# Performance work log

Hardware: AMD Instinct MI355X
Metric: run time of the kernel (lower is better)

Reference implementation:

```python
import jax, jax.numpy as jnp
import numpy as np

GROUPS = 8
EPS = 1e-5


def group_norm(x, gamma, beta):
    # x: [B, C, H, W]; normalize per group over (C/g, H, W)
    B, C, H, W = x.shape
    xg = x.reshape(B, GROUPS, C // GROUPS, H, W)
    mean = xg.mean(axis=(2, 3, 4), keepdims=True)
    var = xg.var(axis=(2, 3, 4), keepdims=True)
    xg = (xg - mean) * jax.lax.rsqrt(var + EPS)
    x = xg.reshape(B, C, H, W)
    return x * gamma[None, :, None, None] + beta[None, :, None, None]


def setup_inputs() -> dict:
    key = jax.random.key(0)
    ks = jax.random.split(key, 6)
    B, C, H, W = 8, 512, 32, 32
    x = jax.random.normal(ks[0], (B, C, H, W), dtype=jnp.float32)
    gn_w = jnp.ones((C,), dtype=jnp.float32)
    gn_b = jnp.zeros((C,), dtype=jnp.float32)
    s = 1.0 / np.sqrt(C)
    qkv_w = jax.random.uniform(ks[1], (3 * C, C), minval=-s, maxval=s, dtype=jnp.float32)
    qkv_b = jax.random.uniform(ks[2], (3 * C,), minval=-s, maxval=s, dtype=jnp.float32)
    proj_w = jax.random.uniform(ks[3], (C, C), minval=-s, maxval=s, dtype=jnp.float32)
    proj_b = jax.random.uniform(ks[4], (C,), minval=-s, maxval=s, dtype=jnp.float32)
    return {"x": x, "gn_w": gn_w, "gn_b": gn_b, "qkv_w": qkv_w,
            "qkv_b": qkv_b, "proj_w": proj_w, "proj_b": proj_b}


def reference(x, gn_w, gn_b, qkv_w, qkv_b, proj_w, proj_b):
    B, C, H, W = x.shape
    xn = group_norm(x, gn_w, gn_b)              # [B,C,H,W] (also the residual)
    xf = xn.reshape(B, C, H * W).transpose(0, 2, 1)  # [B,N,C]
    qkv = jnp.einsum('bnc,dc->bnd', xf, qkv_w) + qkv_b  # [B,N,3C]
    q, k, v = jnp.split(qkv, 3, axis=-1)
    k = jax.nn.softmax(k, axis=-1)              # over channels
    q = jax.nn.softmax(q, axis=-2)              # over tokens
    context = jnp.einsum('bnc,bnd->bcd', k, v)  # [B,C,C]
    out = jnp.einsum('bnc,bcd->bnd', q, context)  # [B,N,C]
    out = jnp.einsum('bnc,dc->bnd', out, proj_w) + proj_b
    out = out.transpose(0, 2, 1).reshape(B, C, H, W)
    return out + xn
```

## Files before the change

### kernel.cpp

```cpp
#include <hip/hip_runtime.h>
#include <hip/hip_bf16.h>
#include <stdint.h>

typedef unsigned short u16;
typedef __attribute__((ext_vector_type(8))) short s16x8;
typedef __attribute__((ext_vector_type(4))) float f32x4;
typedef __attribute__((ext_vector_type(4))) unsigned short u16x4;

static constexpr int B_ = 8, C_ = 512, N_ = 1024, G_ = 8;
static constexpr float EPS = 1e-5f;

static constexpr size_t OFF_XNT  = 0;
static constexpr size_t OFF_Q    = OFF_XNT  + (size_t)B_*N_*C_*2;
static constexpr size_t OFF_K    = OFF_Q    + (size_t)B_*N_*C_*2;
static constexpr size_t OFF_V    = OFF_K    + (size_t)B_*N_*C_*2;
static constexpr size_t OFF_KT   = OFF_V    + (size_t)B_*N_*C_*2;
static constexpr size_t OFF_VT   = OFF_KT   + (size_t)B_*N_*C_*2;
static constexpr size_t OFF_QS   = OFF_VT   + (size_t)B_*N_*C_*2;
static constexpr size_t OFF_CTX  = OFF_QS   + (size_t)B_*N_*C_*2;
static constexpr size_t OFF_MT   = OFF_CTX  + (size_t)B_*C_*C_*2;
static constexpr size_t OFF_WQ   = OFF_MT   + (size_t)B_*C_*C_*2;
static constexpr size_t OFF_WP   = OFF_WQ   + (size_t)3*C_*C_*2;
static constexpr size_t OFF_GNP  = OFF_WP   + (size_t)C_*C_*2;

__device__ __forceinline__ float b2f(u16 u) {
  union { float f; uint32_t i; } x; x.i = ((uint32_t)u) << 16; return x.f;
}
__device__ __forceinline__ u16 f2b(float f) {
  union { float f; uint32_t i; } x; x.f = f;
  return (u16)((x.i + 0x7fffu + ((x.i >> 16) & 1u)) >> 16);
}
#define AS1 __attribute__((address_space(1)))
#define AS3 __attribute__((address_space(3)))
__device__ __forceinline__ void gl2lds16(const void* g, void* l) {
  __builtin_amdgcn_global_load_lds((const AS1 void*)g, (AS3 void*)l, 16, 0, 0);
}

__global__ __launch_bounds__(256) void gn_partial(const float* __restrict__ x,
                                                  float* __restrict__ gnp) {
  int bg = blockIdx.x;
  int chunk = blockIdx.y;
  const float4* p = reinterpret_cast<const float4*>(x + (size_t)bg * 65536 + (size_t)chunk * 8192);
  int tid = threadIdx.x;
  float s = 0.f, sq = 0.f;
#pragma unroll
  for (int i = 0; i < 8; ++i) {
    float4 v = p[i * 256 + tid];
    s  += v.x + v.y + v.z + v.w;
    sq += v.x*v.x + v.y*v.y + v.z*v.z + v.w*v.w;
  }
  for (int off = 32; off; off >>= 1) { s += __shfl_xor(s, off); sq += __shfl_xor(sq, off); }
  __shared__ float red[8];
  int wid = tid >> 6, lane = tid & 63;
  if (lane == 0) { red[wid*2] = s; red[wid*2+1] = sq; }
  __syncthreads();
  if (tid == 0) {
    gnp[(bg*8 + chunk)*2 + 0] = red[0]+red[2]+red[4]+red[6];
    gnp[(bg*8 + chunk)*2 + 1] = red[1]+red[3]+red[5]+red[7];
  }
}

__global__ __launch_bounds__(256) void gn_apply(const float* __restrict__ x,
                                                const float* __restrict__ gw,
                                                const float* __restrict__ gb,
                                                const float* __restrict__ gnp,
                                                u16* __restrict__ xnT) {
  __shared__ float T[64][65];
  int b = blockIdx.x, c0 = blockIdx.y * 64, n0 = blockIdx.z * 64;
  int bg = b * G_ + blockIdx.y;
  float S = 0.f, SQ = 0.f;
#pragma unroll
  for (int i = 0; i < 8; ++i) { S += gnp[(bg*8+i)*2]; SQ += gnp[(bg*8+i)*2+1]; }
  float mean = S * (1.f/65536.f);
  float var  = SQ * (1.f/65536.f) - mean*mean;
  float rstd = rsqrtf(var + EPS);
  int tn = threadIdx.x & 63, tc = threadIdx.x >> 6;
#pragma unroll 4
  for (int it = 0; it < 16; ++it) {
    int cl = it*4 + tc;
    int c = c0 + cl;
    float v = x[((size_t)b*C_ + c)*N_ + n0 + tn];
    T[tn][cl] = (v - mean) * rstd * gw[c] + gb[c];
  }
  __syncthreads();
#pragma unroll
  for (int p = 0; p < 2; ++p) {
    int nl = p*32 + (threadIdx.x >> 3);
    int cs = (threadIdx.x & 7) * 8;
    s16x8 o;
#pragma unroll
    for (int j = 0; j < 8; ++j) o[j] = (short)f2b(T[nl][cs + j]);
    *reinterpret_cast<s16x8*>(&xnT[((size_t)(b*N_ + n0 + nl))*C_ + c0 + cs]) = o;
  }
}

__global__ __launch_bounds__(256) void cvt_w2(const float* __restrict__ w1,
                                              const float* __restrict__ w2,
                                              u16* __restrict__ o1,
                                              u16* __restrict__ o2) {
  int i = blockIdx.x * 256 + threadIdx.x;
  const int n1 = 1536*512/4;
  if (i < n1) {
    float4 v = reinterpret_cast<const float4*>(w1)[i];
    u16x4 r = { f2b(v.x), f2b(v.y), f2b(v.z), f2b(v.w) };
    reinterpret_cast<u16x4*>(o1)[i] = r;
  } else {
    int j = i - n1;
    float4 v = reinterpret_cast<const float4*>(w2)[j];
    u16x4 r = { f2b(v.x), f2b(v.y), f2b(v.z), f2b(v.w) };
    reinterpret_cast<u16x4*>(o2)[j] = r;
  }
}

template<int BM, int BN, int EPI>
__global__ __launch_bounds__(256) void gemm(const u16* __restrict__ A,
                                            const u16* __restrict__ Bm,
                                            int M, int N, int K, int lda, int ldb,
                                            long strideA, long strideB, long strideC,
                                            const float* __restrict__ bias,
                                            void* __restrict__ O0,
                                            const void* __restrict__ R) {
  constexpr int BK = 64;
  constexpr int MI = BM / 32, NI = BN / 32;
  __shared__ u16 As[2][BM*BK];
  __shared__ u16 Bs[2][BN*BK];
  int tid = threadIdx.x, wid = tid >> 6, lane = tid & 63;
  int m0 = blockIdx.x * BM, n0 = blockIdx.y * BN;
  const u16* Ab = A + (size_t)strideA * blockIdx.z;
  const u16* Bp = Bm + (size_t)strideB * blockIdx.z;

  f32x4 acc[MI][NI] = {};
  int wm = (wid >> 1) * (BM/2), wn = (wid & 1) * (BN/2);
  int sr = lane >> 3;
  int sg = (lane & 7) ^ sr;

  auto stage = [&](int buf, int k0) {
#pragma unroll
    for (int t = 0; t < BM/32; ++t) {
      int chunk = wid*(BM/32) + t;
      gl2lds16(Ab + (size_t)(m0 + chunk*8 + sr)*lda + k0 + sg*8,
               (void*)(&As[buf][chunk*512]));
    }
#pragma unroll
    for (int t = 0; t < BN/32; ++t) {
      int chunk = wid*(BN/32) + t;
      gl2lds16(Bp + (size_t)(n0 + chunk*8 + sr)*ldb + k0 + sg*8,
               (void*)(&Bs[buf][chunk*512]));
    }
  };

  int KT = K / BK;
  stage(0, 0);
  __syncthreads();
  int cur = 0;
  for (int kt = 0; kt < KT; ++kt) {
    if (kt + 1 < KT) stage(cur ^ 1, (kt + 1) * BK);
#pragma unroll
    for (int ks = 0; ks < BK; ks += 32) {
      int s = (ks >> 3) + (lane >> 4);
      s16x8 af[MI], bfr[NI];
#pragma unroll
      for (int mi = 0; mi < MI; ++mi) {
        int ar = wm + mi*16 + (lane & 15);
        af[mi] = *reinterpret_cast<const s16x8*>(&As[cur][ar*64 + ((s ^ (ar & 7)) << 3)]);
      }
#pragma unroll
      for (int ni = 0; ni < NI; ++ni) {
        int br = wn + ni*16 + (lane & 15);
        bfr[ni] = *reinterpret_cast<const s16x8*>(&Bs[cur][br*64 + ((s ^ (br & 7)) << 3)]);
      }
#pragma unroll
      for (int mi = 0; mi < MI; ++mi)
#pragma unroll
        for (int ni = 0; ni < NI; ++ni)
          acc[mi][ni] = __builtin_amdgcn_mfma_f32_16x16x32_bf16(af[mi], bfr[ni], acc[mi][ni], 0, 0, 0);
    }
    __syncthreads();
    cur ^= 1;
  }

#pragma unroll
  for (int mi = 0; mi < MI; ++mi) {
#pragma unroll
    for (int ni = 0; ni < NI; ++ni) {
      int col = n0 + wn + ni*16 + (lane & 15);
      if constexpr (EPI == 2) {
        int n = m0 + wm + mi*16 + (lane >> 4)*4;
        int b = blockIdx.z;
        const u16* xr = (const u16*)R + ((size_t)(b*N_ + n))*C_ + col;
        size_t idx = (size_t)b*524288 + (size_t)col*1024 + n;
        float bi = bias[col];
        float4 o;
        o.x = acc[mi][ni][0] + bi + b2f(xr[0]);
        o.y = acc[mi][ni][1] + bi + b2f(xr[512]);
        o.z = acc[mi][ni][2] + bi + b2f(xr[1024]);
        o.w = acc[mi][ni][3] + bi + b2f(xr[1536]);
        *reinterpret_cast<float4*>((float*)O0 + idx) = o;
      } else {
#pragma unroll
        for (int r = 0; r < 4; ++r) {
          int row = m0 + wm + mi*16 + (lane >> 4)*4 + r;
          ((u16*)O0)[(size_t)strideC*blockIdx.z + (size_t)row*N + col] = f2b(acc[mi][ni][r]);
        }
      }
    }
  }
}

__global__ __launch_bounds__(256) void gemm_qkv(const u16* __restrict__ A,
                                                const u16* __restrict__ Bm,
                                                const float* __restrict__ bias,
                                                u16* __restrict__ Oq,
                                                u16* __restrict__ Ok,
                                                u16* __restrict__ Ov) {
  constexpr int BM = 128, BN = 128, BK = 64;
  const int lda = 512, ldb = 512;
  __shared__ u16 As[2][BM*BK];
  __shared__ u16 Bs[2][BN*BK];
  int tid = threadIdx.x, wid = tid >> 6, lane = tid & 63;
  int m0 = blockIdx.x * BM, n0 = blockIdx.y * BN;

  f32x4 acc[4][4] = {};
  int wm = (wid >> 1) * 64, wn = (wid & 1) * 64;
  int sr = lane >> 3;
  int sg = (lane & 7) ^ sr;

  auto stage = [&](int buf, int k0) {
#pragma unroll
    for (int t = 0; t < 4; ++t) {
      int chunk = wid*4 + t;
      gl2lds16(A + (size_t)(m0 + chunk*8 + sr)*lda + k0 + sg*8,
               (void*)(&As[buf][chunk*512]));
      gl2lds16(Bm + (size_t)(n0 + chunk*8 + sr)*ldb + k0 + sg*8,
               (void*)(&Bs[buf][chunk*512]));
    }
  };

  stage(0, 0);
  __syncthreads();
  int cur = 0;
  for (int kt = 0; kt < 8; ++kt) {
    if (kt + 1 < 8) stage(cur ^ 1, (kt + 1) * BK);
#pragma unroll
    for (int ks = 0; ks < BK; ks += 32) {
      int s = (ks >> 3) + (lane >> 4);
      s16x8 af[4], bfr[4];
#pragma unroll
      for (int mi = 0; mi < 4; ++mi) {
        int ar = wm + mi*16 + (lane & 15);
        af[mi] = *reinterpret_cast<const s16x8*>(&As[cur][ar*64 + ((s ^ (ar & 7)) << 3)]);
      }
#pragma unroll
      for (int ni = 0; ni < 4; ++ni) {
        int br = wn + ni*16 + (lane & 15);
        bfr[ni] = *reinterpret_cast<const s16x8*>(&Bs[cur][br*64 + ((s ^ (br & 7)) << 3)]);
      }
#pragma unroll
      for (int mi = 0; mi < 4; ++mi)
#pragma unroll
        for (int ni = 0; ni < 4; ++ni)
          acc[mi][ni] = __builtin_amdgcn_mfma_f32_16x16x32_bf16(af[mi], bfr[ni], acc[mi][ni], 0, 0, 0);
    }
    __syncthreads();
    cur ^= 1;
  }

  u16* Odst; int cbase;
  if (n0 < 512)       { Odst = Oq; cbase = n0; }
  else if (n0 < 1024) { Odst = Ok; cbase = n0 - 512; }
  else                { Odst = Ov; cbase = n0 - 1024; }
#pragma unroll
  for (int mi = 0; mi < 4; ++mi) {
#pragma unroll
    for (int ni = 0; ni < 4; ++ni) {
      int col = n0 + wn + ni*16 + (lane & 15);
      int c   = cbase + wn + ni*16 + (lane & 15);
      float bi = bias[col];
#pragma unroll
      for (int r = 0; r < 4; ++r) {
        int row = m0 + wm + mi*16 + (lane >> 4)*4 + r;
        Odst[(size_t)row*512 + c] = f2b(acc[mi][ni][r] + bi);
      }
    }
  }
}

__global__ __launch_bounds__(256) void kv_transform(const u16* __restrict__ kin,
                                                    const u16* __restrict__ vin,
                                                    u16* __restrict__ kT,
                                                    u16* __restrict__ vT) {
  __shared__ u16 T[32][516];
  int b = blockIdx.x, n0 = blockIdx.y * 32;
  int wid = threadIdx.x >> 6, lane = threadIdx.x & 63;

#pragma unroll
  for (int i = 0; i < 8; ++i) {
    int r = wid * 8 + i;
    const u16* p = kin + ((size_t)(b*N_ + n0 + r))*C_;
    s16x8 raw = reinterpret_cast<const s16x8*>(p)[lane];
    float v[8]; float m = -3e38f;
#pragma unroll
    for (int j = 0; j < 8; ++j) { v[j] = b2f((u16)raw[j]); m = fmaxf(m, v[j]); }
    for (int off = 32; off; off >>= 1) m = fmaxf(m, __shfl_xor(m, off));
    float s = 0.f;
#pragma unroll
    for (int j = 0; j < 8; ++j) { v[j] = __expf(v[j] - m); s += v[j]; }
    for (int off = 32; off; off >>= 1) s += __shfl_xor(s, off);
    float inv = 1.f / s;
    union { s16x8 v8; unsigned long long d[2]; } o;
#pragma unroll
    for (int j = 0; j < 8; ++j) o.v8[j] = (short)f2b(v[j] * inv);
    unsigned long long* dst = reinterpret_cast<unsigned long long*>(&T[r][lane*8]);
    dst[0] = o.d[0]; dst[1] = o.d[1];
  }
  __syncthreads();
#pragma unroll
  for (int h = 0; h < 2; ++h) {
    int c = h*256 + threadIdx.x;
    u16* dst = kT + ((size_t)(b*C_ + c))*N_ + n0;
#pragma unroll
    for (int q4 = 0; q4 < 4; ++q4) {
      s16x8 o;
#pragma unroll
      for (int j = 0; j < 8; ++j) o[j] = (short)T[q4*8 + j][c];
      reinterpret_cast<s16x8*>(dst)[q4] = o;
    }
  }
  __syncthreads();

#pragma unroll
  for (int i = 0; i < 8; ++i) {
    int r = wid * 8 + i;
    const u16* p = vin + ((size_t)(b*N_ + n0 + r))*C_;
    union { s16x8 v8; unsigned long long d[2]; } o;
    o.v8 = reinterpret_cast<const s16x8*>(p)[lane];
    unsigned long long* dst = reinterpret_cast<unsigned long long*>(&T[r][lane*8]);
    dst[0] = o.d[0]; dst[1] = o.d[1];
  }
  __syncthreads();
#pragma unroll
  for (int h = 0; h < 2; ++h) {
    int c = h*256 + threadIdx.x;
    u16* dst = vT + ((size_t)(b*C_ + c))*N_ + n0;
#pragma unroll
    for (int q4 = 0; q4 < 4; ++q4) {
      s16x8 o;
#pragma unroll
      for (int j = 0; j < 8; ++j) o[j] = (short)T[q4*8 + j][c];
      reinterpret_cast<s16x8*>(dst)[q4] = o;
    }
  }
}

__global__ __launch_bounds__(256) void q_softmax(const u16* __restrict__ q,
                                                 u16* __restrict__ qs) {
  int b = blockIdx.x, c0 = blockIdx.y * 32;
  int t = threadIdx.x;
  int cg = t & 3;
  int rw = t >> 2;
  const u16* base = q + (size_t)b*N_*C_ + c0 + cg*8;
  float m[8], s[8];
#pragma unroll
  for (int j = 0; j < 8; ++j) { m[j] = -3e38f; s[j] = 0.f; }
  for (int it = 0; it < 16; ++it) {
    int n = it*64 + rw;
    s16x8 raw = *reinterpret_cast<const s16x8*>(base + (size_t)n*C_);
#pragma unroll
    for (int j = 0; j < 8; ++j) {
      float v = b2f((u16)raw[j]);
      float nm = fmaxf(m[j], v);
      s[j] = s[j]*__expf(m[j] - nm) + __expf(v - nm);
      m[j] = nm;
    }
  }
  __shared__ float Mr[32][65], Sr[32][65];
#pragma unroll
  for (int j = 0; j < 8; ++j) { Mr[cg*8 + j][rw] = m[j]; Sr[cg*8 + j][rw] = s[j]; }
  __syncthreads();
  __shared__ float MS[32][2];
  if (t < 32) {
    float M = -3e38f;
    for (int i = 0; i < 64; ++i) M = fmaxf(M, Mr[t][i]);
    float S = 0.f;
    for (int i = 0; i < 64; ++i) S += Sr[t][i]*__expf(Mr[t][i] - M);
    MS[t][0] = M; MS[t][1] = 1.f / S;
  }
  __syncthreads();
  float Mv[8], Iv[8];
#pragma unroll
  for (int j = 0; j < 8; ++j) { Mv[j] = MS[cg*8 + j][0]; Iv[j] = MS[cg*8 + j][1]; }
  u16* ob = qs + (size_t)b*N_*C_ + c0 + cg*8;
  for (int it = 0; it < 16; ++it) {
    int n = it*64 + rw;
    s16x8 raw = *reinterpret_cast<const s16x8*>(base + (size_t)n*C_);
    s16x8 o;
#pragma unroll
    for (int j = 0; j < 8; ++j)
      o[j] = (short)f2b(__expf(b2f((u16)raw[j]) - Mv[j]) * Iv[j]);
    *reinterpret_cast<s16x8*>(ob + (size_t)n*C_) = o;
  }
}

extern "C" void kernel_launch(void* const* d_in, const int* in_sizes, int n_in,
                              void* d_out, int out_size, void* d_ws, size_t ws_size,
                              hipStream_t stream) {
  (void)in_sizes; (void)n_in; (void)out_size; (void)ws_size;
  const float* x      = (const float*)d_in[0];
  const float* gn_w   = (const float*)d_in[1];
  const float* gn_b   = (const float*)d_in[2];
  const float* qkv_w  = (const float*)d_in[3];
  const float* qkv_b  = (const float*)d_in[4];
  const float* proj_w = (const float*)d_in[5];
  const float* proj_b = (const float*)d_in[6];

  char* ws = (char*)d_ws;
  u16*   xnT  = (u16*)  (ws + OFF_XNT);
  u16*   qb   = (u16*)  (ws + OFF_Q);
  u16*   kb   = (u16*)  (ws + OFF_K);
  u16*   vb   = (u16*)  (ws + OFF_V);
  u16*   kT   = (u16*)  (ws + OFF_KT);
  u16*   vT   = (u16*)  (ws + OFF_VT);
  u16*   qsb  = (u16*)  (ws + OFF_QS);
  u16*   ctx  = (u16*)  (ws + OFF_CTX);
  u16*   mt   = (u16*)  (ws + OFF_MT);
  u16*   wq   = (u16*)  (ws + OFF_WQ);
  u16*   wp   = (u16*)  (ws + OFF_WP);
  float* gnp  = (float*)(ws + OFF_GNP);

  gn_partial<<<dim3(64, 8), 256, 0, stream>>>(x, gnp);
  gn_apply<<<dim3(8, 8, 16), 256, 0, stream>>>(x, gn_w, gn_b, gnp, xnT);

  cvt_w2<<<dim3(1024), 256, 0, stream>>>(qkv_w, proj_w, wq, wp);

  gemm_qkv<<<dim3(64, 12), 256, 0, stream>>>(xnT, wq, qkv_b, qb, kb, vb);

  kv_transform<<<dim3(8, 32), 256, 0, stream>>>(kb, vb, kT, vT);
  q_softmax<<<dim3(8, 16), 256, 0, stream>>>(qb, qsb);

  gemm<64,64,1><<<dim3(8, 8, 8), 256, 0, stream>>>(kT, vT, 512, 512, 1024, 1024, 1024,
                                                   524288, 524288, 262144, nullptr, ctx, nullptr);
  gemm<64,64,1><<<dim3(8, 8, 8), 256, 0, stream>>>(wp, ctx, 512, 512, 512, 512, 512,
                                                   0, 262144, 262144, nullptr, mt, nullptr);
  gemm<64,64,2><<<dim3(16, 8, 8), 256, 0, stream>>>(qsb, mt, 1024, 512, 512, 512, 512,
                                                    524288, 262144, 0, proj_b, (float*)d_out, xnT);
}
```

Baseline: 172.2 us.

## Merge small kernels and retile QKV GEMM to 256x256 with 8 waves

Combines the group-norm partial reduction with the weight conversion, and the k/v softmax-transpose with the q softmax, into single launches dispatched by block index. The QKV projection GEMM is replaced by a 256x256-tile, 512-thread variant with explicit waitcnt-based double buffering and MFMA priority raising. This reduces launch count and increases per-block data reuse, but the larger tile leaves fewer blocks than CUs and uses much more LDS per block.

```diff
diff --git a/kernel.cpp b/kernel.cpp
--- a/kernel.cpp
+++ b/kernel.cpp
@@ -36,27 +36,46 @@
   __builtin_amdgcn_global_load_lds((const AS1 void*)g, (AS3 void*)l, 16, 0, 0);
 }
 
-__global__ __launch_bounds__(256) void gn_partial(const float* __restrict__ x,
-                                                  float* __restrict__ gnp) {
-  int bg = blockIdx.x;
-  int chunk = blockIdx.y;
-  const float4* p = reinterpret_cast<const float4*>(x + (size_t)bg * 65536 + (size_t)chunk * 8192);
-  int tid = threadIdx.x;
-  float s = 0.f, sq = 0.f;
-#pragma unroll
-  for (int i = 0; i < 8; ++i) {
-    float4 v = p[i * 256 + tid];
-    s  += v.x + v.y + v.z + v.w;
-    sq += v.x*v.x + v.y*v.y + v.z*v.z + v.w*v.w;
-  }
-  for (int off = 32; off; off >>= 1) { s += __shfl_xor(s, off); sq += __shfl_xor(sq, off); }
-  __shared__ float red[8];
-  int wid = tid >> 6, lane = tid & 63;
-  if (lane == 0) { red[wid*2] = s; red[wid*2+1] = sq; }
-  __syncthreads();
-  if (tid == 0) {
-    gnp[(bg*8 + chunk)*2 + 0] = red[0]+red[2]+red[4]+red[6];
-    gnp[(bg*8 + chunk)*2 + 1] = red[1]+red[3]+red[5]+red[7];
+__global__ __launch_bounds__(256) void pre_kernel(const float* __restrict__ x,
+                                                  float* __restrict__ gnp,
+                                                  const float* __restrict__ w1,
+                                                  const float* __restrict__ w2,
+                                                  u16* __restrict__ o1,
+                                                  u16* __restrict__ o2) {
+  int bid = blockIdx.x;
+  if (bid < 512) {
+    int bg = bid >> 3, chunk = bid & 7;
+    const float4* p = reinterpret_cast<const float4*>(x + (size_t)bg * 65536 + (size_t)chunk * 8192);
+    int tid = threadIdx.x;
+    float s = 0.f, sq = 0.f;
+#pragma unroll
+    for (int i = 0; i < 8; ++i) {
+      float4 v = p[i * 256 + tid];
+      s  += v.x + v.y + v.z + v.w;
+      sq += v.x*v.x + v.y*v.y + v.z*v.z + v.w*v.w;
+    }
+    for (int off = 32; off; off >>= 1) { s += __shfl_xor(s, off); sq += __shfl_xor(sq, off); }
+    __shared__ float red[8];
+    int wid = tid >> 6, lane = tid & 63;
+    if (lane == 0) { red[wid*2] = s; red[wid*2+1] = sq; }
+    __syncthreads();
+    if (tid == 0) {
+      gnp[(bg*8 + chunk)*2 + 0] = red[0]+red[2]+red[4]+red[6];
+      gnp[(bg*8 + chunk)*2 + 1] = red[1]+red[3]+red[5]+red[7];
+    }
+  } else {
+    int i = (bid - 512) * 256 + threadIdx.x;
+    const int n1 = 1536*512/4;
+    if (i < n1) {
+      float4 v = reinterpret_cast<const float4*>(w1)[i];
+      u16x4 r = { f2b(v.x), f2b(v.y), f2b(v.z), f2b(v.w) };
+      reinterpret_cast<u16x4*>(o1)[i] = r;
+    } else {
+      int j = i - n1;
+      float4 v = reinterpret_cast<const float4*>(w2)[j];
+      u16x4 r = { f2b(v.x), f2b(v.y), f2b(v.z), f2b(v.w) };
+      reinterpret_cast<u16x4*>(o2)[j] = r;
+    }
   }
 }
 
@@ -94,21 +113,101 @@
   }
 }
 
-__global__ __launch_bounds__(256) void cvt_w2(const float* __restrict__ w1,
-                                              const float* __restrict__ w2,
-                                              u16* __restrict__ o1,
-                                              u16* __restrict__ o2) {
-  int i = blockIdx.x * 256 + threadIdx.x;
-  const int n1 = 1536*512/4;
-  if (i < n1) {
-    float4 v = reinterpret_cast<const float4*>(w1)[i];
-    u16x4 r = { f2b(v.x), f2b(v.y), f2b(v.z), f2b(v.w) };
-    reinterpret_cast<u16x4*>(o1)[i] = r;
-  } else {
-    int j = i - n1;
-    float4 v = reinterpret_cast<const float4*>(w2)[j];
-    u16x4 r = { f2b(v.x), f2b(v.y), f2b(v.z), f2b(v.w) };
-    reinterpret_cast<u16x4*>(o2)[j] = r;
+__global__ __launch_bounds__(512, 2) void gemm_qkv8(const u16* __restrict__ A,
+                                                    const u16* __restrict__ Bm,
+                                                    const float* __restrict__ bias,
+                                                    u16* __restrict__ Oq,
+                                                    u16* __restrict__ Ok,
+                                                    u16* __restrict__ Ov) {
+  const int lda = 512, ldb = 512;
+  __shared__ u16 As[2][256*64];
+  __shared__ u16 Bs[2][256*64];
+  int tid = threadIdx.x, wid = tid >> 6, lane = tid & 63;
+  int wr = wid >> 2, wc = wid & 3;
+  int m0 = blockIdx.x * 256, n0 = blockIdx.y * 256;
+
+  f32x4 acc[8][4] = {};
+  int sr = lane >> 3;
+  int sg = (lane & 7) ^ sr;
+
+  auto stage = [&](int buf, int k0) {
+#pragma unroll
+    for (int t = 0; t < 4; ++t) {
+      int chunk = wid*4 + t;
+      gl2lds16(A  + (size_t)(m0 + chunk*8 + sr)*lda + k0 + sg*8,
+               (void*)(&As[buf][chunk*512]));
+      gl2lds16(Bm + (size_t)(n0 + chunk*8 + sr)*ldb + k0 + sg*8,
+               (void*)(&Bs[buf][chunk*512]));
+    }
+  };
+
+  stage(0, 0);
+  int cur = 0;
+  for (int kt = 0; kt < 8; ++kt) {
+    if (kt + 1 < 8) {
+      stage(cur ^ 1, (kt + 1) * 64);
+      asm volatile("s_waitcnt vmcnt(8)" ::: "memory");
+    } else {
+      asm volatile("s_waitcnt vmcnt(0)" ::: "memory");
+    }
+    __builtin_amdgcn_s_barrier();
+    __builtin_amdgcn_sched_barrier(0);
+
+#pragma unroll
+    for (int q = 0; q < 4; ++q) {
+      const int qa = q >> 1, qb = q & 1;
+      s16x8 af[4][2], bfq[2][2];
+#pragma unroll
+      for (int mi2 = 0; mi2 < 4; ++mi2)
+#pragma unroll
+        for (int ks2 = 0; ks2 < 2; ++ks2) {
+          int ar = wr*128 + qa*64 + mi2*16 + (lane & 15);
+          int s  = ks2*4 + (lane >> 4);
+          af[mi2][ks2] = *reinterpret_cast<const s16x8*>(&As[cur][ar*64 + ((s ^ (ar & 7)) << 3)]);
+        }
+#pragma unroll
+      for (int ni2 = 0; ni2 < 2; ++ni2)
+#pragma unroll
+        for (int ks2 = 0; ks2 < 2; ++ks2) {
+          int br = wc*64 + qb*32 + ni2*16 + (lane & 15);
+          int s  = ks2*4 + (lane >> 4);
+          bfq[ni2][ks2] = *reinterpret_cast<const s16x8*>(&Bs[cur][br*64 + ((s ^ (br & 7)) << 3)]);
+        }
+      __builtin_amdgcn_s_setprio(1);
+#pragma unroll
+      for (int mi2 = 0; mi2 < 4; ++mi2)
+#pragma unroll
+        for (int ni2 = 0; ni2 < 2; ++ni2)
+#pragma unroll
+          for (int ks2 = 0; ks2 < 2; ++ks2)
+            acc[qa*4 + mi2][qb*2 + ni2] =
+              __builtin_amdgcn_mfma_f32_16x16x32_bf16(af[mi2][ks2], bfq[ni2][ks2],
+                                                      acc[qa*4 + mi2][qb*2 + ni2], 0, 0, 0);
+      __builtin_amdgcn_s_setprio(0);
+    }
+
+    asm volatile("s_waitcnt lgkmcnt(0)" ::: "memory");
+    __builtin_amdgcn_s_barrier();
+    __builtin_amdgcn_sched_barrier(0);
+    cur ^= 1;
+  }
+
+  u16* Odst; int cbase;
+  if (n0 < 512)       { Odst = Oq; cbase = n0; }
+  else if (n0 < 1024) { Odst = Ok; cbase = n0 - 512; }
+  else                { Odst = Ov; cbase = n0 - 1024; }
+#pragma unroll
+  for (int mi = 0; mi < 8; ++mi) {
+#pragma unroll
+    for (int ni = 0; ni < 4; ++ni) {
+      int cseg = cbase + wc*64 + ni*16 + (lane & 15);
+      float bi = bias[n0 + wc*64 + ni*16 + (lane & 15)];
+#pragma unroll
+      for (int r = 0; r < 4; ++r) {
+        int row = m0 + wr*128 + mi*16 + (lane >> 4)*4 + r;
+        Odst[(size_t)row*512 + cseg] = f2b(acc[mi][ni][r] + bi);
+      }
+    }
   }
 }
 
@@ -207,197 +306,124 @@
   }
 }
 
-__global__ __launch_bounds__(256) void gemm_qkv(const u16* __restrict__ A,
-                                                const u16* __restrict__ Bm,
-                                                const float* __restrict__ bias,
-                                                u16* __restrict__ Oq,
-                                                u16* __restrict__ Ok,
-                                                u16* __restrict__ Ov) {
-  constexpr int BM = 128, BN = 128, BK = 64;
-  const int lda = 512, ldb = 512;
-  __shared__ u16 As[2][BM*BK];
-  __shared__ u16 Bs[2][BN*BK];
-  int tid = threadIdx.x, wid = tid >> 6, lane = tid & 63;
-  int m0 = blockIdx.x * BM, n0 = blockIdx.y * BN;
-
-  f32x4 acc[4][4] = {};
-  int wm = (wid >> 1) * 64, wn = (wid & 1) * 64;
-  int sr = lane >> 3;
-  int sg = (lane & 7) ^ sr;
-
-  auto stage = [&](int buf, int k0) {
-#pragma unroll
-    for (int t = 0; t < 4; ++t) {
-      int chunk = wid*4 + t;
-      gl2lds16(A + (size_t)(m0 + chunk*8 + sr)*lda + k0 + sg*8,
-               (void*)(&As[buf][chunk*512]));
-      gl2lds16(Bm + (size_t)(n0 + chunk*8 + sr)*ldb + k0 + sg*8,
-               (void*)(&Bs[buf][chunk*512]));
-    }
-  };
-
-  stage(0, 0);
-  __syncthreads();
-  int cur = 0;
-  for (int kt = 0; kt < 8; ++kt) {
-    if (kt + 1 < 8) stage(cur ^ 1, (kt + 1) * BK);
-#pragma unroll
-    for (int ks = 0; ks < BK; ks += 32) {
-      int s = (ks >> 3) + (lane >> 4);
-      s16x8 af[4], bfr[4];
-#pragma unroll
-      for (int mi = 0; mi < 4; ++mi) {
-        int ar = wm + mi*16 + (lane & 15);
-        af[mi] = *reinterpret_cast<const s16x8*>(&As[cur][ar*64 + ((s ^ (ar & 7)) << 3)]);
-      }
-#pragma unroll
-      for (int ni = 0; ni < 4; ++ni) {
-        int br = wn + ni*16 + (lane & 15);
-        bfr[ni] = *reinterpret_cast<const s16x8*>(&Bs[cur][br*64 + ((s ^ (br & 7)) << 3)]);
-      }
-#pragma unroll
-      for (int mi = 0; mi < 4; ++mi)
-#pragma unroll
-        for (int ni = 0; ni < 4; ++ni)
-          acc[mi][ni] = __builtin_amdgcn_mfma_f32_16x16x32_bf16(af[mi], bfr[ni], acc[mi][ni], 0, 0, 0);
-    }
-    __syncthreads();
-    cur ^= 1;
-  }
-
-  u16* Odst; int cbase;
-  if (n0 < 512)       { Odst = Oq; cbase = n0; }
-  else if (n0 < 1024) { Odst = Ok; cbase = n0 - 512; }
-  else                { Odst = Ov; cbase = n0 - 1024; }
-#pragma unroll
-  for (int mi = 0; mi < 4; ++mi) {
-#pragma unroll
-    for (int ni = 0; ni < 4; ++ni) {
-      int col = n0 + wn + ni*16 + (lane & 15);
-      int c   = cbase + wn + ni*16 + (lane & 15);
-      float bi = bias[col];
-#pragma unroll
-      for (int r = 0; r < 4; ++r) {
-        int row = m0 + wm + mi*16 + (lane >> 4)*4 + r;
-        Odst[(size_t)row*512 + c] = f2b(acc[mi][ni][r] + bi);
-      }
-    }
-  }
-}
-
-__global__ __launch_bounds__(256) void kv_transform(const u16* __restrict__ kin,
-                                                    const u16* __restrict__ vin,
-                                                    u16* __restrict__ kT,
-                                                    u16* __restrict__ vT) {
-  __shared__ u16 T[32][516];
-  int b = blockIdx.x, n0 = blockIdx.y * 32;
-  int wid = threadIdx.x >> 6, lane = threadIdx.x & 63;
-
-#pragma unroll
-  for (int i = 0; i < 8; ++i) {
-    int r = wid * 8 + i;
-    const u16* p = kin + ((size_t)(b*N_ + n0 + r))*C_;
-    s16x8 raw = reinterpret_cast<const s16x8*>(p)[lane];
-    float v[8]; float m = -3e38f;
-#pragma unroll
-    for (int j = 0; j < 8; ++j) { v[j] = b2f((u16)raw[j]); m = fmaxf(m, v[j]); }
-    for (int off = 32; off; off >>= 1) m = fmaxf(m, __shfl_xor(m, off));
-    float s = 0.f;
-#pragma unroll
-    for (int j = 0; j < 8; ++j) { v[j] = __expf(v[j] - m); s += v[j]; }
-    for (int off = 32; off; off >>= 1) s += __shfl_xor(s, off);
-    float inv = 1.f / s;
-    union { s16x8 v8; unsigned long long d[2]; } o;
-#pragma unroll
-    for (int j = 0; j < 8; ++j) o.v8[j] = (short)f2b(v[j] * inv);
-    unsigned long long* dst = reinterpret_cast<unsigned long long*>(&T[r][lane*8]);
-    dst[0] = o.d[0]; dst[1] = o.d[1];
-  }
-  __syncthreads();
-#pragma unroll
-  for (int h = 0; h < 2; ++h) {
-    int c = h*256 + threadIdx.x;
-    u16* dst = kT + ((size_t)(b*C_ + c))*N_ + n0;
-#pragma unroll
-    for (int q4 = 0; q4 < 4; ++q4) {
+__global__ __launch_bounds__(256) void mid_kernel(const u16* __restrict__ kin,
+                                                  const u16* __restrict__ vin,
+                                                  u16* __restrict__ kT,
+                                                  u16* __restrict__ vT,
+                                                  const u16* __restrict__ q,
+                                                  u16* __restrict__ qs) {
+  __shared__ __align__(16) char smem[33024];
+  int bid = blockIdx.x;
+  if (bid < 256) {
+    u16 (*T)[516] = (u16(*)[516])smem;
+    int b = bid >> 5, n0 = (bid & 31) * 32;
+    int wid = threadIdx.x >> 6, lane = threadIdx.x & 63;
+
+#pragma unroll
+    for (int i = 0; i < 8; ++i) {
+      int r = wid * 8 + i;
+      const u16* p = kin + ((size_t)(b*N_ + n0 + r))*C_;
+      s16x8 raw = reinterpret_cast<const s16x8*>(p)[lane];
+      float v[8]; float m = -3e38f;
+#pragma unroll
+      for (int j = 0; j < 8; ++j) { v[j] = b2f((u16)raw[j]); m = fmaxf(m, v[j]); }
+      for (int off = 32; off; off >>= 1) m = fmaxf(m, __shfl_xor(m, off));
+      float s = 0.f;
+#pragma unroll
+      for (int j = 0; j < 8; ++j) { v[j] = __expf(v[j] - m); s += v[j]; }
+      for (int off = 32; off; off >>= 1) s += __shfl_xor(s, off);
+      float inv = 1.f / s;
+      union { s16x8 v8; unsigned long long d[2]; } o;
+#pragma unroll
+      for (int j = 0; j < 8; ++j) o.v8[j] = (short)f2b(v[j] * inv);
+      unsigned long long* dst = reinterpret_cast<unsigned long long*>(&T[r][lane*8]);
+      dst[0] = o.d[0]; dst[1] = o.d[1];
+    }
+    __syncthreads();
+#pragma unroll
+    for (int h = 0; h < 2; ++h) {
+      int c = h*256 + threadIdx.x;
+      u16* dst = kT + ((size_t)(b*C_ + c))*N_ + n0;
+#pragma unroll
+      for (int q4 = 0; q4 < 4; ++q4) {
+        s16x8 o;
+#pragma unroll
+        for (int j = 0; j < 8; ++j) o[j] = (short)T[q4*8 + j][c];
+        reinterpret_cast<s16x8*>(dst)[q4] = o;
+      }
+    }
+    __syncthreads();
+
+#pragma unroll
+    for (int i = 0; i < 8; ++i) {
+      int r = wid * 8 + i;
+      const u16* p = vin + ((size_t)(b*N_ + n0 + r))*C_;
+      union { s16x8 v8; unsigned long long d[2]; } o;
+      o.v8 = reinterpret_cast<const s16x8*>(p)[lane];
+      unsigned long long* dst = reinterpret_cast<unsigned long long*>(&T[r][lane*8]);
+      dst[0] = o.d[0]; dst[1] = o.d[1];
+    }
+    __syncthreads();
+#pragma unroll
+    for (int h = 0; h < 2; ++h) {
+      int c = h*256 + threadIdx.x;
+      u16* dst = vT + ((size_t)(b*C_ + c))*N_ + n0;
+#pragma unroll
+      for (int q4 = 0; q4 < 4; ++q4) {
+        s16x8 o;
+#pragma unroll
+        for (int j = 0; j < 8; ++j) o[j] = (short)T[q4*8 + j][c];
+        reinterpret_cast<s16x8*>(dst)[q4] = o;
+      }
+    }
+  } else {
+    float (*Mr)[65] = (float(*)[65])smem;
+    float (*Sr)[65] = (float(*)[65])(smem + 8320);
+    float (*MS)[2]  = (float(*)[2]) (smem + 16640);
+    int j2 = bid - 256;
+    int b = j2 >> 4, c0 = (j2 & 15) * 32;
+    int t = threadIdx.x;
+    int cg = t & 3;
+    int rw = t >> 2;
+    const u16* base = q + (size_t)b*N_*C_ + c0 + cg*8;
+    float m[8], s[8];
+#pragma unroll
+    for (int j = 0; j < 8; ++j) { m[j] = -3e38f; s[j] = 0.f; }
+    for (int it = 0; it < 16; ++it) {
+      int n = it*64 + rw;
+      s16x8 raw = *reinterpret_cast<const s16x8*>(base + (size_t)n*C_);
+#pragma unroll
+      for (int j = 0; j < 8; ++j) {
+        float v = b2f((u16)raw[j]);
+        float nm = fmaxf(m[j], v);
+        s[j] = s[j]*__expf(m[j] - nm) + __expf(v - nm);
+        m[j] = nm;
+      }
+    }
+#pragma unroll
+    for (int j = 0; j < 8; ++j) { Mr[cg*8 + j][rw] = m[j]; Sr[cg*8 + j][rw] = s[j]; }
+    __syncthreads();
+    if (t < 32) {
+      float M = -3e38f;
+      for (int i = 0; i < 64; ++i) M = fmaxf(M, Mr[t][i]);
+      float S = 0.f;
+      for (int i = 0; i < 64; ++i) S += Sr[t][i]*__expf(Mr[t][i] - M);
+      MS[t][0] = M; MS[t][1] = 1.f / S;
+    }
+    __syncthreads();
+    float Mv[8], Iv[8];
+#pragma unroll
+    for (int j = 0; j < 8; ++j) { Mv[j] = MS[cg*8 + j][0]; Iv[j] = MS[cg*8 + j][1]; }
+    u16* ob = qs + (size_t)b*N_*C_ + c0 + cg*8;
+    for (int it = 0; it < 16; ++it) {
+      int n = it*64 + rw;
+      s16x8 raw = *reinterpret_cast<const s16x8*>(base + (size_t)n*C_);
       s16x8 o;
 #pragma unroll
-      for (int j = 0; j < 8; ++j) o[j] = (short)T[q4*8 + j][c];
-      reinterpret_cast<s16x8*>(dst)[q4] = o;
-    }
-  }
-  __syncthreads();
-
-#pragma unroll
-  for (int i = 0; i < 8; ++i) {
-    int r = wid * 8 + i;
-    const u16* p = vin + ((size_t)(b*N_ + n0 + r))*C_;
-    union { s16x8 v8; unsigned long long d[2]; } o;
-    o.v8 = reinterpret_cast<const s16x8*>(p)[lane];
-    unsigned long long* dst = reinterpret_cast<unsigned long long*>(&T[r][lane*8]);
-    dst[0] = o.d[0]; dst[1] = o.d[1];
-  }
-  __syncthreads();
-#pragma unroll
-  for (int h = 0; h < 2; ++h) {
-    int c = h*256 + threadIdx.x;
-    u16* dst = vT + ((size_t)(b*C_ + c))*N_ + n0;
-#pragma unroll
-    for (int q4 = 0; q4 < 4; ++q4) {
-      s16x8 o;
-#pragma unroll
-      for (int j = 0; j < 8; ++j) o[j] = (short)T[q4*8 + j][c];
-      reinterpret_cast<s16x8*>(dst)[q4] = o;
-    }
-  }
-}
-
-__global__ __launch_bounds__(256) void q_softmax(const u16* __restrict__ q,
-                                                 u16* __restrict__ qs) {
-  int b = blockIdx.x, c0 = blockIdx.y * 32;
-  int t = threadIdx.x;
-  int cg = t & 3;
-  int rw = t >> 2;
-  const u16* base = q + (size_t)b*N_*C_ + c0 + cg*8;
-  float m[8], s[8];
-#pragma unroll
-  for (int j = 0; j < 8; ++j) { m[j] = -3e38f; s[j] = 0.f; }
-  for (int it = 0; it < 16; ++it) {
-    int n = it*64 + rw;
-    s16x8 raw = *reinterpret_cast<const s16x8*>(base + (size_t)n*C_);
-#pragma unroll
-    for (int j = 0; j < 8; ++j) {
-      float v = b2f((u16)raw[j]);
-      float nm = fmaxf(m[j], v);
-      s[j] = s[j]*__expf(m[j] - nm) + __expf(v - nm);
-      m[j] = nm;
-    }
-  }
-  __shared__ float Mr[32][65], Sr[32][65];
-#pragma unroll
-  for (int j = 0; j < 8; ++j) { Mr[cg*8 + j][rw] = m[j]; Sr[cg*8 + j][rw] = s[j]; }
-  __syncthreads();
-  __shared__ float MS[32][2];
-  if (t < 32) {
-    float M = -3e38f;
-    for (int i = 0; i < 64; ++i) M = fmaxf(M, Mr[t][i]);
-    float S = 0.f;
-    for (int i = 0; i < 64; ++i) S += Sr[t][i]*__expf(Mr[t][i] - M);
-    MS[t][0] = M; MS[t][1] = 1.f / S;
-  }
-  __syncthreads();
-  float Mv[8], Iv[8];
-#pragma unroll
-  for (int j = 0; j < 8; ++j) { Mv[j] = MS[cg*8 + j][0]; Iv[j] = MS[cg*8 + j][1]; }
-  u16* ob = qs + (size_t)b*N_*C_ + c0 + cg*8;
-  for (int it = 0; it < 16; ++it) {
-    int n = it*64 + rw;
-    s16x8 raw = *reinterpret_cast<const s16x8*>(base + (size_t)n*C_);
-    s16x8 o;
-#pragma unroll
-    for (int j = 0; j < 8; ++j)
-      o[j] = (short)f2b(__expf(b2f((u16)raw[j]) - Mv[j]) * Iv[j]);
-    *reinterpret_cast<s16x8*>(ob + (size_t)n*C_) = o;
+      for (int j = 0; j < 8; ++j)
+        o[j] = (short)f2b(__expf(b2f((u16)raw[j]) - Mv[j]) * Iv[j]);
+      *reinterpret_cast<s16x8*>(ob + (size_t)n*C_) = o;
+    }
   }
 }
 
@@ -427,15 +453,12 @@
   u16*   wp   = (u16*)  (ws + OFF_WP);
   float* gnp  = (float*)(ws + OFF_GNP);
 
-  gn_partial<<<dim3(64, 8), 256, 0, stream>>>(x, gnp);
+  pre_kernel<<<dim3(1536), 256, 0, stream>>>(x, gnp, qkv_w, proj_w, wq, wp);
   gn_apply<<<dim3(8, 8, 16), 256, 0, stream>>>(x, gn_w, gn_b, gnp, xnT);
 
-  cvt_w2<<<dim3(1024), 256, 0, stream>>>(qkv_w, proj_w, wq, wp);
-
-  gemm_qkv<<<dim3(64, 12), 256, 0, stream>>>(xnT, wq, qkv_b, qb, kb, vb);
-
-  kv_transform<<<dim3(8, 32), 256, 0, stream>>>(kb, vb, kT, vT);
-  q_softmax<<<dim3(8, 16), 256, 0, stream>>>(qb, qsb);
+  gemm_qkv8<<<dim3(32, 6), 512, 0, stream>>>(xnT, wq, qkv_b, qb, kb, vb);
+
+  mid_kernel<<<dim3(384), 256, 0, stream>>>(kb, vb, kT, vT, qb, qsb);
 
   gemm<64,64,1><<<dim3(8, 8, 8), 256, 0, stream>>>(kT, vT, 512, 512, 1024, 1024, 1024,
                                                    524288, 524288, 262144, nullptr, ctx, nullptr);
```

New measurement: 163.1 us. 5.3% less time.
